# Optimization experiments

Measured on AMD Instinct MI355X. Metric: run time of the kernel, lower is better.

Reference implementation:

```python
import jax, jax.numpy as jnp
import numpy as np

B, E, N, M = 512, 1024, 1024, 128
EPS = 1e-16


def setup_inputs() -> dict:
    key = jax.random.key(0)
    k1, k2, k3, k4 = jax.random.split(key, 4)
    embeddings = jax.random.normal(k1, (B, E), dtype=jnp.float32)
    w_prev = jax.random.uniform(k2, (B, N), dtype=jnp.float32)
    w_prev = w_prev / jnp.sum(w_prev, axis=1, keepdims=True)  # valid attention over N slots
    memory = jax.random.normal(k3, (B, N, M), dtype=jnp.float32)
    W = jax.random.normal(k4, (E, M + 6), dtype=jnp.float32) * (1.4 / np.sqrt(0.5 * (E + M + 6)))
    b = jnp.zeros((M + 6,), dtype=jnp.float32)
    return {"embeddings": embeddings, "w_prev": w_prev, "memory": memory, "W": W, "b": b}


def reference(embeddings, w_prev, memory, W, b):
    # Dense projection to (k | beta | g | s | y), widths (M, 1, 1, 3, 1)
    params = embeddings @ W + b  # [B, M+6]
    k = params[:, :M]                       # content key [B, M]
    beta = jax.nn.softplus(params[:, M:M + 1])   # key strength >= 0
    g = jax.nn.sigmoid(params[:, M + 1:M + 2])   # interpolation gate in (0,1)
    s = jax.nn.softmax(params[:, M + 2:M + 5], axis=1)  # shift weights [B, 3]
    y = 1.0 + jax.nn.softplus(params[:, M + 5:M + 6])   # sharpening >= 1

    # Content addressing: cosine similarity of key vs each memory row
    dot = jnp.einsum('bm,bnm->bn', k, memory)  # [B, N]
    k_norm = jnp.linalg.norm(k, axis=1, keepdims=True)          # [B, 1]
    m_norm = jnp.linalg.norm(memory, axis=2)                    # [B, N]
    cos = dot / (k_norm * m_norm + EPS)
    w_c = jax.nn.softmax(beta * cos, axis=1)  # [B, N]

    # Interpolate with previous weighting
    w_g = g * w_c + (1.0 - g) * w_prev

    # Circular convolution with 3-tap shift kernel (shifts -1, 0, +1)
    w_tilde = (s[:, 0:1] * jnp.roll(w_g, 1, axis=1)
               + s[:, 1:2] * w_g
               + s[:, 2:3] * jnp.roll(w_g, -1, axis=1))

    # Sharpen
    w_pow = jnp.power(w_tilde + EPS, y)
    w = w_pow / jnp.sum(w_pow, axis=1, keepdims=True)  # memory_locations [B, N]

    # Memory read: weighted sum of rows
    memory_data = jnp.einsum('bn,bnm->bm', w, memory)  # [B, M]
    return (memory_data, w)
```

## Files before the change

kernel.cpp:

```cpp
#include <hip/hip_runtime.h>
#include <hip/hip_bf16.h>

#define B_ 512
#define E_ 1024
#define N_ 1024
#define M_ 128
#define P_ 134

#define RLO 24
#define LLO 18

__device__ __forceinline__ float softplus_f(float x) {
    return fmaxf(x, 0.f) + log1pf(expf(-fabsf(x)));
}

__global__ __launch_bounds__(1024) void k_fused(
    const float* __restrict__ emb, const float* __restrict__ W,
    const float* __restrict__ bias, const float* __restrict__ w_prev,
    const float* __restrict__ mem,
    float* __restrict__ out_md, float* __restrict__ out_w)
{
    __shared__ float se[E_];
    __shared__ float partial[4][136];
    __shared__ float sp[136];
    __shared__ float sscal[8];
    __shared__ float zbuf[N_];
    __shared__ float wgbuf[N_];
    __shared__ float red[16];
    __shared__ float4 acc16[16][32];
    __shared__ float cache[6][32][M_];

    const int b    = blockIdx.x;
    const int t    = threadIdx.x;
    const int wid  = t >> 6;
    const int lane = t & 63;
    const int half = lane >> 5, q = lane & 31;

    for (int i = t; i < E_; i += 1024) se[i] = emb[b * E_ + i];
    __syncthreads();
    if (t < 536) {
        const int seg = t / 134;
        const int col = t - seg * 134;
        const int e0 = seg * 256;
        const float* wcol = W + col;
        float a0 = 0.f, a1 = 0.f, a2 = 0.f, a3 = 0.f;
        #pragma unroll 4
        for (int e = 0; e < 256; e += 4) {
            a0 = fmaf(se[e0 + e + 0], wcol[(size_t)(e0 + e + 0) * P_], a0);
            a1 = fmaf(se[e0 + e + 1], wcol[(size_t)(e0 + e + 1) * P_], a1);
            a2 = fmaf(se[e0 + e + 2], wcol[(size_t)(e0 + e + 2) * P_], a2);
            a3 = fmaf(se[e0 + e + 3], wcol[(size_t)(e0 + e + 3) * P_], a3);
        }
        partial[seg][col] = (a0 + a1) + (a2 + a3);
    }
    __syncthreads();
    if (t < P_)
        sp[t] = bias[t] + ((partial[0][t] + partial[1][t]) + (partial[2][t] + partial[3][t]));
    __syncthreads();
    if (t < 64) {
        float v = sp[t] * sp[t] + sp[t + 64] * sp[t + 64];
        #pragma unroll
        for (int m = 1; m < 64; m <<= 1) v += __shfl_xor(v, m);
        if (t == 0) sscal[6] = sqrtf(v);
    }
    if (t == 64) {
        sscal[0] = softplus_f(sp[M_ + 0]);
        sscal[1] = 1.f / (1.f + expf(-sp[M_ + 1]));
        float a0 = sp[M_ + 2], a1 = sp[M_ + 3], a2 = sp[M_ + 4];
        float mx = fmaxf(a0, fmaxf(a1, a2));
        float e0 = expf(a0 - mx), e1 = expf(a1 - mx), e2 = expf(a2 - mx);
        float inv = 1.f / (e0 + e1 + e2);
        sscal[2] = e0 * inv; sscal[3] = e1 * inv; sscal[4] = e2 * inv;
        sscal[5] = 1.f + softplus_f(sp[M_ + 5]);
    }
    __syncthreads();

    const float4 k4   = *(const float4*)&sp[q * 4];
    const float  kn   = sscal[6];
    const float  beta = sscal[0];
    const float  g    = sscal[1];
    const float  s0   = sscal[2];
    const float  s1   = sscal[3];
    const float  s2   = sscal[4];
    const float  y    = sscal[5];

    const float* base = mem + ((size_t)b * N_ + wid * 64 + half) * M_ + q * 4;
    float4 rc[8];

    #pragma unroll 6
    for (int i = 0; i < LLO; ++i) {
        const float4 v = *(const float4*)(base + (size_t)i * 2 * M_);
        float dot = v.x * k4.x + v.y * k4.y + v.z * k4.z + v.w * k4.w;
        float sq  = v.x * v.x + v.y * v.y + v.z * v.z + v.w * v.w;
        #pragma unroll
        for (int m = 1; m < 32; m <<= 1) {
            dot += __shfl_xor(dot, m);
            sq  += __shfl_xor(sq,  m);
        }
        if (q == 0)
            zbuf[wid * 64 + 2 * i + half] = beta * dot / (kn * sqrtf(sq) + 1e-16f);
    }
    #pragma unroll
    for (int i = LLO; i < RLO; ++i) {
        const float4 v = *(const float4*)(base + (size_t)i * 2 * M_);
        *(float4*)&cache[i - LLO][wid * 2 + half][q * 4] = v;
        float dot = v.x * k4.x + v.y * k4.y + v.z * k4.z + v.w * k4.w;
        float sq  = v.x * v.x + v.y * v.y + v.z * v.z + v.w * v.w;
        #pragma unroll
        for (int m = 1; m < 32; m <<= 1) {
            dot += __shfl_xor(dot, m);
            sq  += __shfl_xor(sq,  m);
        }
        if (q == 0)
            zbuf[wid * 64 + 2 * i + half] = beta * dot / (kn * sqrtf(sq) + 1e-16f);
    }
    #pragma unroll
    for (int ii = 0; ii < 8; ++ii) {
        const int i = RLO + ii;
        const float4 v = *(const float4*)(base + (size_t)i * 2 * M_);
        rc[ii] = v;
        float dot = v.x * k4.x + v.y * k4.y + v.z * k4.z + v.w * k4.w;
        float sq  = v.x * v.x + v.y * v.y + v.z * v.z + v.w * v.w;
        #pragma unroll
        for (int m = 1; m < 32; m <<= 1) {
            dot += __shfl_xor(dot, m);
            sq  += __shfl_xor(sq,  m);
        }
        if (q == 0)
            zbuf[wid * 64 + 2 * i + half] = beta * dot / (kn * sqrtf(sq) + 1e-16f);
    }
    __syncthreads();

    float zv = zbuf[t];
    float v = zv;
    #pragma unroll
    for (int m = 1; m < 64; m <<= 1) v = fmaxf(v, __shfl_xor(v, m));
    if (lane == 0) red[wid] = v;
    __syncthreads();
    float mx = red[0];
    #pragma unroll
    for (int j = 1; j < 16; ++j) mx = fmaxf(mx, red[j]);
    float ev = expf(zv - mx);
    v = ev;
    #pragma unroll
    for (int m = 1; m < 64; m <<= 1) v += __shfl_xor(v, m);
    __syncthreads();
    if (lane == 0) red[wid] = v;
    __syncthreads();
    float esum = 0.f;
    #pragma unroll
    for (int j = 0; j < 16; ++j) esum += red[j];
    float wc = ev / esum;
    wgbuf[t] = g * wc + (1.f - g) * w_prev[b * N_ + t];
    __syncthreads();
    float wt = s0 * wgbuf[(t - 1) & (N_ - 1)] + s1 * wgbuf[t] + s2 * wgbuf[(t + 1) & (N_ - 1)];
    float wp = powf(wt + 1e-16f, y);
    v = wp;
    #pragma unroll
    for (int m = 1; m < 64; m <<= 1) v += __shfl_xor(v, m);
    __syncthreads();
    if (lane == 0) red[wid] = v;
    __syncthreads();
    float psum = 0.f;
    #pragma unroll
    for (int j = 0; j < 16; ++j) psum += red[j];
    float wfin = wp / psum;
    zbuf[t] = wfin;
    out_w[b * N_ + t] = wfin;
    __syncthreads();

    float4 acc = make_float4(0.f, 0.f, 0.f, 0.f);
    #pragma unroll
    for (int ii = 7; ii >= 0; --ii) {
        float wv = zbuf[wid * 64 + 2 * (RLO + ii) + half];
        acc.x = fmaf(wv, rc[ii].x, acc.x);
        acc.y = fmaf(wv, rc[ii].y, acc.y);
        acc.z = fmaf(wv, rc[ii].z, acc.z);
        acc.w = fmaf(wv, rc[ii].w, acc.w);
    }
    #pragma unroll
    for (int i = RLO - 1; i >= LLO; --i) {
        float wv = zbuf[wid * 64 + 2 * i + half];
        const float4 mv = *(const float4*)&cache[i - LLO][wid * 2 + half][q * 4];
        acc.x = fmaf(wv, mv.x, acc.x);
        acc.y = fmaf(wv, mv.y, acc.y);
        acc.z = fmaf(wv, mv.z, acc.z);
        acc.w = fmaf(wv, mv.w, acc.w);
    }
    #pragma unroll 6
    for (int i = LLO - 1; i >= 0; --i) {
        float wv = zbuf[wid * 64 + 2 * i + half];
        const float4 mv = *(const float4*)(base + (size_t)i * 2 * M_);
        acc.x = fmaf(wv, mv.x, acc.x);
        acc.y = fmaf(wv, mv.y, acc.y);
        acc.z = fmaf(wv, mv.z, acc.z);
        acc.w = fmaf(wv, mv.w, acc.w);
    }
    acc.x += __shfl_xor(acc.x, 32);
    acc.y += __shfl_xor(acc.y, 32);
    acc.z += __shfl_xor(acc.z, 32);
    acc.w += __shfl_xor(acc.w, 32);
    if (lane < 32) acc16[wid][q] = acc;
    __syncthreads();
    if (t < 32) {
        float4 s = acc16[0][t];
        #pragma unroll
        for (int j = 1; j < 16; ++j) {
            float4 u = acc16[j][t];
            s.x += u.x; s.y += u.y; s.z += u.z; s.w += u.w;
        }
        *(float4*)&out_md[b * M_ + t * 4] = s;
    }
}

extern "C" void kernel_launch(void* const* d_in, const int* in_sizes, int n_in,
                              void* d_out, int out_size, void* d_ws, size_t ws_size,
                              hipStream_t stream) {
    const float* emb    = (const float*)d_in[0];
    const float* w_prev = (const float*)d_in[1];
    const float* mem    = (const float*)d_in[2];
    const float* W      = (const float*)d_in[3];
    const float* bias   = (const float*)d_in[4];

    float* out_md = (float*)d_out;
    float* out_w  = (float*)d_out + B_ * M_;

    k_fused<<<B_, 1024, 0, stream>>>(emb, W, bias, w_prev, mem, out_md, out_w);
}
```

Measured before the change: 406.7 us.

## Shrink blocks to 512 threads, drop LDS/register row caching, re-read memory

```diff
diff --git a/kernel.cpp b/kernel.cpp
--- a/kernel.cpp
+++ b/kernel.cpp
@@ -7,45 +7,43 @@
 #define M_ 128
 #define P_ 134
 
-#define RLO 24
-#define LLO 18
-
 __device__ __forceinline__ float softplus_f(float x) {
     return fmaxf(x, 0.f) + log1pf(expf(-fabsf(x)));
 }
 
-__global__ __launch_bounds__(1024) void k_fused(
+__global__ __launch_bounds__(512, 4) void k_fused(
     const float* __restrict__ emb, const float* __restrict__ W,
     const float* __restrict__ bias, const float* __restrict__ w_prev,
     const float* __restrict__ mem,
     float* __restrict__ out_md, float* __restrict__ out_w)
 {
     __shared__ float se[E_];
-    __shared__ float partial[4][136];
+    __shared__ float partial[2][136];
     __shared__ float sp[136];
     __shared__ float sscal[8];
     __shared__ float zbuf[N_];
     __shared__ float wgbuf[N_];
-    __shared__ float red[16];
-    __shared__ float4 acc16[16][32];
-    __shared__ float cache[6][32][M_];
+    __shared__ float red[8];
+    __shared__ float accw[8][M_];
 
     const int b    = blockIdx.x;
     const int t    = threadIdx.x;
     const int wid  = t >> 6;
     const int lane = t & 63;
-    const int half = lane >> 5, q = lane & 31;
-
-    for (int i = t; i < E_; i += 1024) se[i] = emb[b * E_ + i];
-    __syncthreads();
-    if (t < 536) {
+    const int c    = lane & 7;
+    const int rg   = lane >> 3;
+
+    se[t] = emb[b * E_ + t];
+    se[t + 512] = emb[b * E_ + t + 512];
+    __syncthreads();
+    if (t < 268) {
         const int seg = t / 134;
         const int col = t - seg * 134;
-        const int e0 = seg * 256;
+        const int e0 = seg * 512;
         const float* wcol = W + col;
         float a0 = 0.f, a1 = 0.f, a2 = 0.f, a3 = 0.f;
         #pragma unroll 4
-        for (int e = 0; e < 256; e += 4) {
+        for (int e = 0; e < 512; e += 4) {
             a0 = fmaf(se[e0 + e + 0], wcol[(size_t)(e0 + e + 0) * P_], a0);
             a1 = fmaf(se[e0 + e + 1], wcol[(size_t)(e0 + e + 1) * P_], a1);
             a2 = fmaf(se[e0 + e + 2], wcol[(size_t)(e0 + e + 2) * P_], a2);
@@ -54,8 +52,7 @@
         partial[seg][col] = (a0 + a1) + (a2 + a3);
     }
     __syncthreads();
-    if (t < P_)
-        sp[t] = bias[t] + ((partial[0][t] + partial[1][t]) + (partial[2][t] + partial[3][t]));
+    if (t < P_) sp[t] = bias[t] + partial[0][t] + partial[1][t];
     __syncthreads();
     if (t < 64) {
         float v = sp[t] * sp[t] + sp[t + 64] * sp[t + 64];
@@ -75,73 +72,54 @@
     }
     __syncthreads();
 
-    const float4 k4   = *(const float4*)&sp[q * 4];
-    const float  kn   = sscal[6];
-    const float  beta = sscal[0];
-    const float  g    = sscal[1];
-    const float  s0   = sscal[2];
-    const float  s1   = sscal[3];
-    const float  s2   = sscal[4];
-    const float  y    = sscal[5];
-
-    const float* base = mem + ((size_t)b * N_ + wid * 64 + half) * M_ + q * 4;
-    float4 rc[8];
-
-    #pragma unroll 6
-    for (int i = 0; i < LLO; ++i) {
-        const float4 v = *(const float4*)(base + (size_t)i * 2 * M_);
-        float dot = v.x * k4.x + v.y * k4.y + v.z * k4.z + v.w * k4.w;
-        float sq  = v.x * v.x + v.y * v.y + v.z * v.z + v.w * v.w;
+    const float kn   = sscal[6];
+    const float beta = sscal[0];
+    const float g    = sscal[1];
+    const float s0   = sscal[2];
+    const float s1   = sscal[3];
+    const float s2   = sscal[4];
+    const float y    = sscal[5];
+
+    const float4 kf0 = *(const float4*)&sp[c * 16 + 0];
+    const float4 kf1 = *(const float4*)&sp[c * 16 + 4];
+    const float4 kf2 = *(const float4*)&sp[c * 16 + 8];
+    const float4 kf3 = *(const float4*)&sp[c * 16 + 12];
+
+    const float* rowbase = mem + ((size_t)b * N_ + wid * 128 + rg) * M_ + c * 16;
+
+    #pragma unroll 4
+    for (int i = 0; i < 16; ++i) {
+        const float4* p = (const float4*)(rowbase + (size_t)i * 8 * M_);
+        const float4 v0 = p[0], v1 = p[1], v2 = p[2], v3 = p[3];
+        float dot = v0.x * kf0.x + v0.y * kf0.y + v0.z * kf0.z + v0.w * kf0.w;
+        float sq  = v0.x * v0.x + v0.y * v0.y + v0.z * v0.z + v0.w * v0.w;
+        dot += v1.x * kf1.x + v1.y * kf1.y + v1.z * kf1.z + v1.w * kf1.w;
+        sq  += v1.x * v1.x + v1.y * v1.y + v1.z * v1.z + v1.w * v1.w;
+        dot += v2.x * kf2.x + v2.y * kf2.y + v2.z * kf2.z + v2.w * kf2.w;
+        sq  += v2.x * v2.x + v2.y * v2.y + v2.z * v2.z + v2.w * v2.w;
+        dot += v3.x * kf3.x + v3.y * kf3.y + v3.z * kf3.z + v3.w * kf3.w;
+        sq  += v3.x * v3.x + v3.y * v3.y + v3.z * v3.z + v3.w * v3.w;
         #pragma unroll
-        for (int m = 1; m < 32; m <<= 1) {
+        for (int m = 1; m < 8; m <<= 1) {
             dot += __shfl_xor(dot, m);
             sq  += __shfl_xor(sq,  m);
         }
-        if (q == 0)
-            zbuf[wid * 64 + 2 * i + half] = beta * dot / (kn * sqrtf(sq) + 1e-16f);
-    }
-    #pragma unroll
-    for (int i = LLO; i < RLO; ++i) {
-        const float4 v = *(const float4*)(base + (size_t)i * 2 * M_);
-        *(float4*)&cache[i - LLO][wid * 2 + half][q * 4] = v;
-        float dot = v.x * k4.x + v.y * k4.y + v.z * k4.z + v.w * k4.w;
-        float sq  = v.x * v.x + v.y * v.y + v.z * v.z + v.w * v.w;
-        #pragma unroll
-        for (int m = 1; m < 32; m <<= 1) {
-            dot += __shfl_xor(dot, m);
-            sq  += __shfl_xor(sq,  m);
-        }
-        if (q == 0)
-            zbuf[wid * 64 + 2 * i + half] = beta * dot / (kn * sqrtf(sq) + 1e-16f);
-    }
-    #pragma unroll
-    for (int ii = 0; ii < 8; ++ii) {
-        const int i = RLO + ii;
-        const float4 v = *(const float4*)(base + (size_t)i * 2 * M_);
-        rc[ii] = v;
-        float dot = v.x * k4.x + v.y * k4.y + v.z * k4.z + v.w * k4.w;
-        float sq  = v.x * v.x + v.y * v.y + v.z * v.z + v.w * v.w;
-        #pragma unroll
-        for (int m = 1; m < 32; m <<= 1) {
-            dot += __shfl_xor(dot, m);
-            sq  += __shfl_xor(sq,  m);
-        }
-        if (q == 0)
-            zbuf[wid * 64 + 2 * i + half] = beta * dot / (kn * sqrtf(sq) + 1e-16f);
-    }
-    __syncthreads();
-
-    float zv = zbuf[t];
-    float v = zv;
+        if (c == 0)
+            zbuf[wid * 128 + i * 8 + rg] = beta * dot / (kn * sqrtf(sq) + 1e-16f);
+    }
+    __syncthreads();
+
+    const float z0 = zbuf[t], z1 = zbuf[t + 512];
+    float v = fmaxf(z0, z1);
     #pragma unroll
     for (int m = 1; m < 64; m <<= 1) v = fmaxf(v, __shfl_xor(v, m));
     if (lane == 0) red[wid] = v;
     __syncthreads();
     float mx = red[0];
     #pragma unroll
-    for (int j = 1; j < 16; ++j) mx = fmaxf(mx, red[j]);
-    float ev = expf(zv - mx);
-    v = ev;
+    for (int j = 1; j < 8; ++j) mx = fmaxf(mx, red[j]);
+    const float e0 = expf(z0 - mx), e1 = expf(z1 - mx);
+    v = e0 + e1;
     #pragma unroll
     for (int m = 1; m < 64; m <<= 1) v += __shfl_xor(v, m);
     __syncthreads();
@@ -149,13 +127,16 @@
     __syncthreads();
     float esum = 0.f;
     #pragma unroll
-    for (int j = 0; j < 16; ++j) esum += red[j];
-    float wc = ev / esum;
-    wgbuf[t] = g * wc + (1.f - g) * w_prev[b * N_ + t];
-    __syncthreads();
-    float wt = s0 * wgbuf[(t - 1) & (N_ - 1)] + s1 * wgbuf[t] + s2 * wgbuf[(t + 1) & (N_ - 1)];
-    float wp = powf(wt + 1e-16f, y);
-    v = wp;
+    for (int j = 0; j < 8; ++j) esum += red[j];
+    const float einv = 1.f / esum;
+    wgbuf[t]       = g * (e0 * einv) + (1.f - g) * w_prev[b * N_ + t];
+    wgbuf[t + 512] = g * (e1 * einv) + (1.f - g) * w_prev[b * N_ + t + 512];
+    __syncthreads();
+    const float wt0 = s0 * wgbuf[(t - 1) & (N_ - 1)] + s1 * wgbuf[t] + s2 * wgbuf[(t + 1) & (N_ - 1)];
+    const float wt1 = s0 * wgbuf[(t + 511) & (N_ - 1)] + s1 * wgbuf[t + 512] + s2 * wgbuf[(t + 513) & (N_ - 1)];
+    const float wp0 = powf(wt0 + 1e-16f, y);
+    const float wp1 = powf(wt1 + 1e-16f, y);
+    v = wp0 + wp1;
     #pragma unroll
     for (int m = 1; m < 64; m <<= 1) v += __shfl_xor(v, m);
     __syncthreads();
@@ -163,53 +144,51 @@
     __syncthreads();
     float psum = 0.f;
     #pragma unroll
-    for (int j = 0; j < 16; ++j) psum += red[j];
-    float wfin = wp / psum;
-    zbuf[t] = wfin;
-    out_w[b * N_ + t] = wfin;
-    __syncthreads();
-
-    float4 acc = make_float4(0.f, 0.f, 0.f, 0.f);
-    #pragma unroll
-    for (int ii = 7; ii >= 0; --ii) {
-        float wv = zbuf[wid * 64 + 2 * (RLO + ii) + half];
-        acc.x = fmaf(wv, rc[ii].x, acc.x);
-        acc.y = fmaf(wv, rc[ii].y, acc.y);
-        acc.z = fmaf(wv, rc[ii].z, acc.z);
-        acc.w = fmaf(wv, rc[ii].w, acc.w);
-    }
-    #pragma unroll
-    for (int i = RLO - 1; i >= LLO; --i) {
-        float wv = zbuf[wid * 64 + 2 * i + half];
-        const float4 mv = *(const float4*)&cache[i - LLO][wid * 2 + half][q * 4];
-        acc.x = fmaf(wv, mv.x, acc.x);
-        acc.y = fmaf(wv, mv.y, acc.y);
-        acc.z = fmaf(wv, mv.z, acc.z);
-        acc.w = fmaf(wv, mv.w, acc.w);
-    }
-    #pragma unroll 6
-    for (int i = LLO - 1; i >= 0; --i) {
-        float wv = zbuf[wid * 64 + 2 * i + half];
-        const float4 mv = *(const float4*)(base + (size_t)i * 2 * M_);
-        acc.x = fmaf(wv, mv.x, acc.x);
-        acc.y = fmaf(wv, mv.y, acc.y);
-        acc.z = fmaf(wv, mv.z, acc.z);
-        acc.w = fmaf(wv, mv.w, acc.w);
-    }
-    acc.x += __shfl_xor(acc.x, 32);
-    acc.y += __shfl_xor(acc.y, 32);
-    acc.z += __shfl_xor(acc.z, 32);
-    acc.w += __shfl_xor(acc.w, 32);
-    if (lane < 32) acc16[wid][q] = acc;
-    __syncthreads();
-    if (t < 32) {
-        float4 s = acc16[0][t];
+    for (int j = 0; j < 8; ++j) psum += red[j];
+    const float pinv = 1.f / psum;
+    const float wf0 = wp0 * pinv, wf1 = wp1 * pinv;
+    zbuf[t] = wf0;       out_w[b * N_ + t] = wf0;
+    zbuf[t + 512] = wf1; out_w[b * N_ + t + 512] = wf1;
+    __syncthreads();
+
+    float4 a0 = {0,0,0,0}, a1 = {0,0,0,0}, a2 = {0,0,0,0}, a3 = {0,0,0,0};
+    #pragma unroll 4
+    for (int i = 0; i < 16; ++i) {
+        const float wv = zbuf[wid * 128 + i * 8 + rg];
+        const float4* p = (const float4*)(rowbase + (size_t)i * 8 * M_);
+        const float4 v0 = p[0], v1 = p[1], v2 = p[2], v3 = p[3];
+        a0.x = fmaf(wv, v0.x, a0.x); a0.y = fmaf(wv, v0.y, a0.y);
+        a0.z = fmaf(wv, v0.z, a0.z); a0.w = fmaf(wv, v0.w, a0.w);
+        a1.x = fmaf(wv, v1.x, a1.x); a1.y = fmaf(wv, v1.y, a1.y);
+        a1.z = fmaf(wv, v1.z, a1.z); a1.w = fmaf(wv, v1.w, a1.w);
+        a2.x = fmaf(wv, v2.x, a2.x); a2.y = fmaf(wv, v2.y, a2.y);
+        a2.z = fmaf(wv, v2.z, a2.z); a2.w = fmaf(wv, v2.w, a2.w);
+        a3.x = fmaf(wv, v3.x, a3.x); a3.y = fmaf(wv, v3.y, a3.y);
+        a3.z = fmaf(wv, v3.z, a3.z); a3.w = fmaf(wv, v3.w, a3.w);
+    }
+    #pragma unroll
+    for (int m = 8; m < 64; m <<= 1) {
+        a0.x += __shfl_xor(a0.x, m); a0.y += __shfl_xor(a0.y, m);
+        a0.z += __shfl_xor(a0.z, m); a0.w += __shfl_xor(a0.w, m);
+        a1.x += __shfl_xor(a1.x, m); a1.y += __shfl_xor(a1.y, m);
+        a1.z += __shfl_xor(a1.z, m); a1.w += __shfl_xor(a1.w, m);
+        a2.x += __shfl_xor(a2.x, m); a2.y += __shfl_xor(a2.y, m);
+        a2.z += __shfl_xor(a2.z, m); a2.w += __shfl_xor(a2.w, m);
+        a3.x += __shfl_xor(a3.x, m); a3.y += __shfl_xor(a3.y, m);
+        a3.z += __shfl_xor(a3.z, m); a3.w += __shfl_xor(a3.w, m);
+    }
+    if (rg == 0) {
+        *(float4*)&accw[wid][c * 16 + 0]  = a0;
+        *(float4*)&accw[wid][c * 16 + 4]  = a1;
+        *(float4*)&accw[wid][c * 16 + 8]  = a2;
+        *(float4*)&accw[wid][c * 16 + 12] = a3;
+    }
+    __syncthreads();
+    if (t < M_) {
+        float s = accw[0][t];
         #pragma unroll
-        for (int j = 1; j < 16; ++j) {
-            float4 u = acc16[j][t];
-            s.x += u.x; s.y += u.y; s.z += u.z; s.w += u.w;
-        }
-        *(float4*)&out_md[b * M_ + t * 4] = s;
+        for (int j = 1; j < 8; ++j) s += accw[j][t];
+        out_md[b * M_ + t] = s;
     }
 }
 
@@ -225,5 +204,5 @@
     float* out_md = (float*)d_out;
     float* out_w  = (float*)d_out + B_ * M_;
 
-    k_fused<<<B_, 1024, 0, stream>>>(emb, W, bias, w_prev, mem, out_md, out_w);
+    k_fused<<<B_, 512, 0, stream>>>(emb, W, bias, w_prev, mem, out_md, out_w);
 }
```

Result: slower. 431.8 us (+6.2%).
